# Kernel optimization log

Hardware: AMD Instinct MI355X
Metric: run time of the kernel (lower is better)

## Reference

```python
import jax, jax.numpy as jnp
import numpy as np

# Conv2d_mvm config (matches init_kwargs): the bit-sliced crossbar MVM is a
# fixed-point emulation of an exact stride-1 conv2d with padding=1, no bias.
C_IN, C_OUT, K, H, W, PAD = 16, 16, 3, 1024, 1024, 1


def setup_inputs() -> dict:
    key = jax.random.key(0)
    kx, kw = jax.random.split(key)
    x = jax.random.normal(kx, (1, C_IN, H, W), dtype=jnp.float32)
    # kaiming_uniform-style init for the conv weight
    fan_in = C_IN * K * K
    bound = 1.0 / np.sqrt(fan_in)
    weight = jax.random.uniform(kw, (C_OUT, C_IN, K, K), dtype=jnp.float32,
                                minval=-bound, maxval=bound)
    return {"x": x, "weight": weight}


def reference(x, weight):
    # Ideal math of the bit-sliced crossbar MVM: per output pixel, the
    # flattened (C_in*K*K) receptive field dotted with each flattened filter.
    out = jax.lax.conv_general_dilated(
        x, weight,
        window_strides=(1, 1),
        padding=((PAD, PAD), (PAD, PAD)),
        dimension_numbers=("NCHW", "OIHW", "NCHW"),
    )
    # Original forward returns (C_out, H_out, W_out) with batch=1 assumed.
    return out[0]
```

## Files before the change

### kernel.cpp

```cpp
#include <hip/hip_runtime.h>


#define H 1024
#define W 1024
#define HW (H * W)
#define TW 64
#define TH 8
#define LROWS 10
#define LPITCH 2112
#define LDS_BYTES (LROWS * LPITCH)

typedef __bf16 bf16x8 __attribute__((ext_vector_type(8)));
typedef float f32x4 __attribute__((ext_vector_type(4)));
typedef unsigned short ushort8 __attribute__((ext_vector_type(8)));
typedef unsigned int uint4v __attribute__((ext_vector_type(4)));

__device__ __host__ inline unsigned short f2bf(float f) {
  unsigned u = __builtin_bit_cast(unsigned, f);
  return (unsigned short)((u + 0x7fffu + ((u >> 16) & 1u)) >> 16);
}

__global__ __launch_bounds__(256) void conv_prep(const float* __restrict__ w,
                                                 unsigned short* __restrict__ wA) {
  int i = blockIdx.x * 256 + threadIdx.x;
  if (i >= 5 * 64 * 8) return;
  int j = i & 7;
  int l = (i >> 3) & 63;
  int p = i >> 9;
  int k = (l >> 4) * 8 + j;
  int t = 2 * p + (k >> 4);
  int ci = k & 15;
  int co = l & 15;
  float v = (t <= 8) ? w[co * 144 + ci * 9 + t] : 0.f;
  wA[i] = f2bf(v);
}

__global__ __launch_bounds__(256, 5) void conv_mfma(
    const float* __restrict__ x, const unsigned short* __restrict__ wA,
    float* __restrict__ out) {
  __shared__ __align__(16) char lds[LDS_BYTES];

  const int tid  = threadIdx.x;
  const int lane = tid & 63;
  const int wave = tid >> 6;
  const int m = lane & 15;
  const int q = lane >> 4;
  const int colbase = blockIdx.x * TW;
  const int rowbase = blockIdx.y * TH;

  if (tid < 180) {
    const int ly  = tid / 18;
    const int qx  = tid - ly * 18;
    const int gy  = rowbase - 1 + ly;
    const int gx0 = colbase - 4 + 4 * qx;
    const bool rowok = (unsigned)gy < (unsigned)H;
    const int gyc  = gy < 0 ? 0 : (gy > H - 1 ? H - 1 : gy);
    const int gx0c = gx0 < 0 ? 0 : (gx0 > W - 4 ? W - 4 : gx0);
    const float* xb = x + gyc * W + gx0c;

    float fm[4];
    int lok[4];
    int lb[4];
    int swz[4];
#pragma unroll
    for (int i = 0; i < 4; ++i) {
      const int gx = gx0 + i;
      fm[i] = (rowok && (unsigned)gx < (unsigned)W) ? 1.f : 0.f;
      const int lx = gx - (colbase - 1);
      lok[i] = (unsigned)lx < 66u;
      lb[i]  = ly * LPITCH + lx * 32;
      swz[i] = ((lx >> 2) & 3) << 4;
    }
#pragma unroll
    for (int h = 0; h < 2; ++h) {
      f32x4 L[8];
#pragma unroll
      for (int c = 0; c < 8; ++c)
        L[c] = *(const f32x4*)(xb + (h * 8 + c) * HW);
#pragma unroll
      for (int i = 0; i < 4; ++i) {
        if (lok[i]) {
          uint4v d;
#pragma unroll
          for (int p = 0; p < 4; ++p) {
            const unsigned lo = f2bf(L[2 * p][i] * fm[i]);
            const unsigned hi = f2bf(L[2 * p + 1][i] * fm[i]);
            d[p] = lo | (hi << 16);
          }
          *(uint4v*)(lds + ((lb[i] + h * 16) ^ swz[i])) = d;
        }
      }
    }
  }

  ushort8 wU[5];
#pragma unroll
  for (int p = 0; p < 5; ++p)
    wU[p] = *(const ushort8*)&wA[(p * 64 + lane) * 8];

  int baseaddr[5];
#pragma unroll
  for (int p = 0; p < 5; ++p) {
    int t = 2 * p + (q >> 1);
    int ky = 0, kx = 0;
    if (t <= 8) { ky = t / 3; kx = t - ky * 3; }
    int col = m + kx;
    int b = ky * LPITCH + col * 32 + (q & 1) * 16;
    b ^= ((col >> 2) & 3) << 4;
    baseaddr[p] = b + wave * 2 * LPITCH;
  }

  __syncthreads();

#pragma unroll
  for (int r = 0; r < 2; ++r) {
#pragma unroll
    for (int g = 0; g < 4; ++g) {
      f32x4 acc = {0.f, 0.f, 0.f, 0.f};
#pragma unroll
      for (int p = 0; p < 5; ++p) {
        ushort8 bU = *(const ushort8*)(lds + (baseaddr[p] + r * LPITCH + g * 512));
        acc = __builtin_amdgcn_mfma_f32_16x16x32_bf16(
            __builtin_bit_cast(bf16x8, bU),
            __builtin_bit_cast(bf16x8, wU[p]),
            acc, 0, 0, 0);
      }
      const int y  = rowbase + wave * 2 + r;
      const int x0 = colbase + g * 16 + q * 4;
      *(f32x4*)(out + m * HW + y * W + x0) = acc;
    }
  }
}

extern "C" void kernel_launch(void* const* d_in, const int* in_sizes, int n_in,
                              void* d_out, int out_size, void* d_ws, size_t ws_size,
                              hipStream_t stream) {
  const float* x = (const float*)d_in[0];
  const float* w = (const float*)d_in[1];
  float* out = (float*)d_out;
  unsigned short* wA = (unsigned short*)d_ws;

  conv_prep<<<10, 256, 0, stream>>>(w, wA);

  dim3 grid(W / TW, H / TH);
  conv_mfma<<<grid, 256, 0, stream>>>(x, wA, out);
}
```

Measured before the change: 43.19 us.

## Process two row tiles per block with register-prefetched input for next tile

```diff
diff --git a/kernel.cpp b/kernel.cpp
--- a/kernel.cpp
+++ b/kernel.cpp
@@ -6,6 +6,7 @@
 #define HW (H * W)
 #define TW 64
 #define TH 8
+#define NT 2
 #define LROWS 10
 #define LPITCH 2112
 #define LDS_BYTES (LROWS * LPITCH)
@@ -35,7 +36,7 @@
   wA[i] = f2bf(v);
 }
 
-__global__ __launch_bounds__(256, 5) void conv_mfma(
+__global__ __launch_bounds__(256, 4) void conv_mfma(
     const float* __restrict__ x, const unsigned short* __restrict__ wA,
     float* __restrict__ out) {
   __shared__ __align__(16) char lds[LDS_BYTES];
@@ -45,51 +46,42 @@
   const int wave = tid >> 6;
   const int m = lane & 15;
   const int q = lane >> 4;
-  const int colbase = blockIdx.x * TW;
-  const int rowbase = blockIdx.y * TH;
+  const int colbase  = blockIdx.x * TW;
+  const int rowbase0 = blockIdx.y * (TH * NT);
 
-  if (tid < 180) {
-    const int ly  = tid / 18;
+  const bool stager = tid < 180;
+  int ly = 0;
+  const float* xcol = x;
+  float cmask[4];
+  int lok[4], lb[4];
+  if (stager) {
+    ly = tid / 18;
     const int qx  = tid - ly * 18;
-    const int gy  = rowbase - 1 + ly;
     const int gx0 = colbase - 4 + 4 * qx;
-    const bool rowok = (unsigned)gy < (unsigned)H;
-    const int gyc  = gy < 0 ? 0 : (gy > H - 1 ? H - 1 : gy);
     const int gx0c = gx0 < 0 ? 0 : (gx0 > W - 4 ? W - 4 : gx0);
-    const float* xb = x + gyc * W + gx0c;
-
-    float fm[4];
-    int lok[4];
-    int lb[4];
-    int swz[4];
+    xcol = x + gx0c;
 #pragma unroll
     for (int i = 0; i < 4; ++i) {
       const int gx = gx0 + i;
-      fm[i] = (rowok && (unsigned)gx < (unsigned)W) ? 1.f : 0.f;
+      cmask[i] = ((unsigned)gx < (unsigned)W) ? 1.f : 0.f;
       const int lx = gx - (colbase - 1);
       lok[i] = (unsigned)lx < 66u;
-      lb[i]  = ly * LPITCH + lx * 32;
-      swz[i] = ((lx >> 2) & 3) << 4;
+      const int b = ly * LPITCH + lx * 32;
+      lb[i] = b ^ (((lx >> 2) & 3) << 4);
     }
+  }
+
+  f32x4 L[16];
+  float rowm;
+  {
+    const int gy = rowbase0 - 1 + ly;
+    rowm = ((unsigned)gy < (unsigned)H) ? 1.f : 0.f;
+    const int gyc = gy < 0 ? 0 : (gy > H - 1 ? H - 1 : gy);
+    const float* xb = xcol + gyc * W;
+    if (stager) {
 #pragma unroll
-    for (int h = 0; h < 2; ++h) {
-      f32x4 L[8];
-#pragma unroll
-      for (int c = 0; c < 8; ++c)
-        L[c] = *(const f32x4*)(xb + (h * 8 + c) * HW);
-#pragma unroll
-      for (int i = 0; i < 4; ++i) {
-        if (lok[i]) {
-          uint4v d;
-#pragma unroll
-          for (int p = 0; p < 4; ++p) {
-            const unsigned lo = f2bf(L[2 * p][i] * fm[i]);
-            const unsigned hi = f2bf(L[2 * p + 1][i] * fm[i]);
-            d[p] = lo | (hi << 16);
-          }
-          *(uint4v*)(lds + ((lb[i] + h * 16) ^ swz[i])) = d;
-        }
-      }
+      for (int c = 0; c < 16; ++c)
+        L[c] = *(const f32x4*)(xb + c * HW);
     }
   }
 
@@ -110,25 +102,65 @@
     baseaddr[p] = b + wave * 2 * LPITCH;
   }
 
-  __syncthreads();
+#pragma unroll
+  for (int t = 0; t < NT; ++t) {
+    if (stager) {
+#pragma unroll
+      for (int h = 0; h < 2; ++h) {
+#pragma unroll
+        for (int i = 0; i < 4; ++i) {
+          if (lok[i]) {
+            const float fm = rowm * cmask[i];
+            uint4v d;
+#pragma unroll
+            for (int p = 0; p < 4; ++p) {
+              const unsigned lo = f2bf(L[h * 8 + 2 * p][i] * fm);
+              const unsigned hi = f2bf(L[h * 8 + 2 * p + 1][i] * fm);
+              d[p] = lo | (hi << 16);
+            }
+            *(uint4v*)(lds + (lb[i] ^ (h << 4)));
+            *(uint4v*)(lds + (lb[i] ^ (h << 4))) = d;
+          }
+        }
+      }
+    }
 
+    if (t + 1 < NT) {
+      const int gy = rowbase0 + (t + 1) * TH - 1 + ly;
+      const float nrowm = ((unsigned)gy < (unsigned)H) ? 1.f : 0.f;
+      const int gyc = gy < 0 ? 0 : (gy > H - 1 ? H - 1 : gy);
+      const float* xb = xcol + gyc * W;
+      if (stager) {
 #pragma unroll
-  for (int r = 0; r < 2; ++r) {
+        for (int c = 0; c < 16; ++c)
+          L[c] = *(const f32x4*)(xb + c * HW);
+      }
+      rowm = nrowm;
+    }
+
+    __syncthreads();
+
+    const int rowbase = rowbase0 + t * TH;
 #pragma unroll
-    for (int g = 0; g < 4; ++g) {
-      f32x4 acc = {0.f, 0.f, 0.f, 0.f};
+    for (int r = 0; r < 2; ++r) {
 #pragma unroll
-      for (int p = 0; p < 5; ++p) {
-        ushort8 bU = *(const ushort8*)(lds + (baseaddr[p] + r * LPITCH + g * 512));
-        acc = __builtin_amdgcn_mfma_f32_16x16x32_bf16(
-            __builtin_bit_cast(bf16x8, bU),
-            __builtin_bit_cast(bf16x8, wU[p]),
-            acc, 0, 0, 0);
+      for (int g = 0; g < 4; ++g) {
+        f32x4 acc = {0.f, 0.f, 0.f, 0.f};
+#pragma unroll
+        for (int p = 0; p < 5; ++p) {
+          ushort8 bU = *(const ushort8*)(lds + (baseaddr[p] + r * LPITCH + g * 512));
+          acc = __builtin_amdgcn_mfma_f32_16x16x32_bf16(
+              __builtin_bit_cast(bf16x8, bU),
+              __builtin_bit_cast(bf16x8, wU[p]),
+              acc, 0, 0, 0);
+        }
+        const int y  = rowbase + wave * 2 + r;
+        const int x0 = colbase + g * 16 + q * 4;
+        *(f32x4*)(out + m * HW + y * W + x0) = acc;
       }
-      const int y  = rowbase + wave * 2 + r;
-      const int x0 = colbase + g * 16 + q * 4;
-      *(f32x4*)(out + m * HW + y * W + x0) = acc;
     }
+
+    if (t + 1 < NT) __syncthreads();
   }
 }
 
@@ -142,6 +174,6 @@
 
   conv_prep<<<10, 256, 0, stream>>>(w, wA);
 
-  dim3 grid(W / TW, H / TH);
+  dim3 grid(W / TW, H / (TH * NT));
   conv_mfma<<<grid, 256, 0, stream>>>(x, wA, out);
 }
```

Result: slower. 44.40 us (+2.8%).
